# Optimization experiments

Hardware: AMD Instinct MI355X
Metric: run time of the kernel (lower is better)

The kernel has to match this reference:

```python
import jax, jax.numpy as jnp
import numpy as np
import math

B, TSRC, TTGT, DM, DI, H = 2, 2048, 2048, 1024, 1024, 16
DH = DI // H
LN_EPS = 1e-5


def setup_inputs() -> dict:
    key = jax.random.key(0)
    ks = iter(jax.random.split(key, 40))
    def p(*shape):
        return jax.random.normal(next(ks), shape, jnp.float32) * 0.02
    inp = {
        "enc_out_vecs": jax.random.normal(next(ks), (B, TSRC, DM), jnp.float32),
        "output_vecs": jax.random.normal(next(ks), (B, TTGT, DM), jnp.float32),
    }
    for tag in ("dd", "ed"):
        inp["Wq_" + tag] = p(DM, DI); inp["bq_" + tag] = jnp.zeros((DI,), jnp.float32)
        inp["Wk_" + tag] = p(DM, DI); inp["bk_" + tag] = jnp.zeros((DI,), jnp.float32)
        inp["Wv_" + tag] = p(DM, DI); inp["bv_" + tag] = jnp.zeros((DI,), jnp.float32)
        inp["Wo_" + tag] = p(DI, DM); inp["bo_" + tag] = jnp.zeros((DM,), jnp.float32)
        inp["W1_" + tag] = p(DM, 2 * DM); inp["b1_" + tag] = jnp.zeros((2 * DM,), jnp.float32)
        inp["W2_" + tag] = p(2 * DM, DM); inp["b2_" + tag] = jnp.zeros((DM,), jnp.float32)
        inp["g1_" + tag] = jnp.ones((DM,), jnp.float32); inp["be1_" + tag] = jnp.zeros((DM,), jnp.float32)
        inp["g2_" + tag] = jnp.ones((DM,), jnp.float32); inp["be2_" + tag] = jnp.zeros((DM,), jnp.float32)
    return inp


def _ln(x, g, b):
    m = jnp.mean(x, axis=-1, keepdims=True)
    v = jnp.var(x, axis=-1, keepdims=True)
    return (x - m) * jax.lax.rsqrt(v + LN_EPS) * g + b


def _mha(xq, xkv, Wq, bq, Wk, bk, Wv, bv, causal):
    Bb, Tq, _ = xq.shape
    Tk = xkv.shape[1]
    q = (xq @ Wq + bq).reshape(Bb, Tq, H, DH)
    k = (xkv @ Wk + bk).reshape(Bb, Tk, H, DH)
    v = (xkv @ Wv + bv).reshape(Bb, Tk, H, DH)
    s = jnp.einsum("bqhd,bkhd->bhqk", q, k) / math.sqrt(DH)
    if causal:
        mask = jnp.where(jnp.arange(Tk)[None, :] > jnp.arange(Tq)[:, None], -jnp.inf, 0.0)
        s = s + mask
    w = jax.nn.softmax(s, axis=-1)
    return jnp.einsum("bhqk,bkhd->bqhd", w, v).reshape(Bb, Tq, H * DH)


def reference(enc_out_vecs, output_vecs,
              Wq_dd, bq_dd, Wk_dd, bk_dd, Wv_dd, bv_dd, Wo_dd, bo_dd,
              W1_dd, b1_dd, W2_dd, b2_dd, g1_dd, be1_dd, g2_dd, be2_dd,
              Wq_ed, bq_ed, Wk_ed, bk_ed, Wv_ed, bv_ed, Wo_ed, bo_ed,
              W1_ed, b1_ed, W2_ed, b2_ed, g1_ed, be1_ed, g2_ed, be2_ed):
    # masked self-attention over decoder inputs
    x = output_vecs
    a = _mha(x, x, Wq_dd, bq_dd, Wk_dd, bk_dd, Wv_dd, bv_dd, causal=True)
    x = _ln(a @ Wo_dd + bo_dd + x, g1_dd, be1_dd)
    x = _ln(x + jax.nn.relu(x @ W1_dd + b1_dd) @ W2_dd + b2_dd, g2_dd, be2_dd)
    # cross attention against encoder outputs
    a = _mha(x, enc_out_vecs, Wq_ed, bq_ed, Wk_ed, bk_ed, Wv_ed, bv_ed, causal=False)
    x = _ln(a @ Wo_ed + bo_ed + x, g1_ed, be1_ed)
    x = _ln(jax.nn.relu(x @ W1_ed + b1_ed) @ W2_ed + b2_ed + x, g2_ed, be2_ed)
    return x
```

## Files before the change

### kernel.cpp

```cpp
#include <hip/hip_runtime.h>
#include <stdint.h>

#define DEV __device__ __forceinline__
typedef unsigned short u16;
typedef __attribute__((ext_vector_type(8))) short bf16x8;
typedef __attribute__((ext_vector_type(4))) float f32x4;

#define AS1 __attribute__((address_space(1)))
#define AS3 __attribute__((address_space(3)))
#define WAITVM0 asm volatile("s_waitcnt vmcnt(0)" ::: "memory")
#define QSCALE 0.18033688011112042f

DEV u16 f2bf(float f) {
  union { float f; uint32_t u; } x; x.f = f;
  uint32_t r = x.u + 0x7fffu + ((x.u >> 16) & 1u);
  return (u16)(r >> 16);
}

DEV uint32_t cvt_pk_bf16(float a, float b) {
  uint32_t r;
  asm("v_cvt_pk_bf16_f32 %0, %1, %2" : "=v"(r) : "v"(a), "v"(b));
  return r;
}

__global__ __launch_bounds__(256) void k_cvt2(const float* __restrict__ a, const float* __restrict__ bsrc,
                                              u16* __restrict__ oa, u16* __restrict__ ob, int n4) {
  int i = blockIdx.x * blockDim.x + threadIdx.x;
  const float* s;
  u16* o;
  int k;
  if (i < n4) { s = a; o = oa; k = i; }
  else        { s = bsrc; o = ob; k = i - n4; }
  float4 v = reinterpret_cast<const float4*>(s)[k];
  reinterpret_cast<ushort4*>(o)[k] = make_ushort4(f2bf(v.x), f2bf(v.y), f2bf(v.z), f2bf(v.w));
}

struct WTJob { const float* W; u16* WT; int K, M, msh, start; };
struct WTJobs { WTJob j[12]; };

__global__ void k_wT_all(WTJobs jobs) {
  __shared__ float tile[32][33];
  int b = blockIdx.x;
  int i = 0;
#pragma unroll
  for (int t = 1; t < 12; ++t)
    if (b >= jobs.j[t].start) i = t;
  const WTJob J = jobs.j[i];
  int rel = b - J.start;
  int m0 = (rel & ((1 << J.msh) - 1)) << 5;
  int k0 = (rel >> J.msh) << 5;
  int tx = threadIdx.x, ty = threadIdx.y;
#pragma unroll
  for (int q = 0; q < 4; ++q)
    tile[ty + q * 8][tx] = J.W[(size_t)(k0 + ty + q * 8) * J.M + m0 + tx];
  __syncthreads();
#pragma unroll
  for (int q = 0; q < 4; ++q)
    J.WT[(size_t)(m0 + ty + q * 8) * J.K + k0 + tx] = f2bf(tile[tx][ty + q * 8]);
}

template<int R>
DEV void stage_tile(const u16* __restrict__ g, int strideElems, u16* lds, int tid, int wv) {
#pragma unroll
  for (int t = 0; t < R / 32; ++t) {
    int idx = t * 256 + tid;
    int row = idx >> 3;
    int b = (idx & 7) << 4;
    int sb = b ^ ((row & 7) << 4);
    const char* src = (const char*)g + (size_t)row * strideElems * 2 + sb;
    char* dst = (char*)lds + (size_t)(t * 256 + wv * 64) * 16;
    __builtin_amdgcn_global_load_lds((const AS1 void*)src, (AS3 void*)dst, 16, 0, 0);
  }
}

DEV bf16x8 lds_frag(const u16* lds, int row, int kel) {
  int off = row * 128 + ((kel * 2) ^ ((row & 7) << 4));
  return *(const bf16x8*)((const char*)lds + off);
}

template<int JT, int MODE>
__global__ __launch_bounds__(256) void k_gemm(const u16* __restrict__ A, int lda,
                                              const u16* __restrict__ BT,
                                              const float* __restrict__ bias,
                                              void* __restrict__ C, int ldc, int K) {
  constexpr int BN = JT * 32;
  __shared__ __align__(16) u16 A_lds[2][128 * 64];
  __shared__ __align__(16) u16 B_lds[2][BN * 64];
  const int tid = threadIdx.x, lane = tid & 63, wv = tid >> 6;
  const int wm = wv >> 1, wn = wv & 1;
  const int nwg = gridDim.x * gridDim.y;
  const int flat = blockIdx.y * gridDim.x + blockIdx.x;
  const int sw = (flat & 7) * (nwg >> 3) + (flat >> 3);
  const int bx = sw % gridDim.x, by = sw / gridDim.x;
  const int bm0 = by * 128, bn0 = bx * BN;
  const int lr = lane & 15, lk = (lane >> 4) * 8, r0 = (lane >> 4) * 4;

  f32x4 acc[4][JT];
#pragma unroll
  for (int i = 0; i < 4; ++i)
#pragma unroll
    for (int j = 0; j < JT; ++j) acc[i][j] = f32x4{0.f, 0.f, 0.f, 0.f};

  stage_tile<128>(A + (size_t)bm0 * lda, lda, A_lds[0], tid, wv);
  stage_tile<BN>(BT + (size_t)bn0 * K, K, B_lds[0], tid, wv);
  WAITVM0;
  __builtin_amdgcn_s_barrier();

  int cur = 0;
  for (int k0 = 0; k0 < K; k0 += 64) {
    if (k0 + 64 < K) {
      stage_tile<128>(A + (size_t)bm0 * lda + k0 + 64, lda, A_lds[cur ^ 1], tid, wv);
      stage_tile<BN>(BT + (size_t)bn0 * K + k0 + 64, K, B_lds[cur ^ 1], tid, wv);
    }
#pragma unroll
    for (int kk = 0; kk < 2; ++kk) {
      bf16x8 af[4], bfr[JT];
#pragma unroll
      for (int i = 0; i < 4; ++i) af[i] = lds_frag(A_lds[cur], wm * 64 + i * 16 + lr, kk * 32 + lk);
#pragma unroll
      for (int j = 0; j < JT; ++j) bfr[j] = lds_frag(B_lds[cur], wn * (JT * 16) + j * 16 + lr, kk * 32 + lk);
#pragma unroll
      for (int i = 0; i < 4; ++i)
#pragma unroll
        for (int j = 0; j < JT; ++j)
          acc[i][j] = __builtin_amdgcn_mfma_f32_16x16x32_bf16(af[i], bfr[j], acc[i][j], 0, 0, 0);
    }
    WAITVM0;
    __builtin_amdgcn_s_barrier();
    cur ^= 1;
  }

#pragma unroll
  for (int j = 0; j < JT; ++j) {
    int col = bn0 + wn * (JT * 16) + j * 16 + lr;
    float bv = bias[col];
#pragma unroll
    for (int i = 0; i < 4; ++i) {
      int rowb = bm0 + wm * 64 + i * 16 + r0;
      if constexpr (MODE == 0) {
#pragma unroll
        for (int r = 0; r < 4; ++r)
          ((float*)C)[(size_t)(rowb + r) * ldc + col] = acc[i][j][r] + bv;
      } else {
#pragma unroll
        for (int r = 0; r < 4; ++r) {
          float v = fmaxf(acc[i][j][r] + bv, 0.f);
          ((u16*)C)[(size_t)(rowb + r) * ldc + col] = f2bf(v);
        }
      }
    }
  }
}

__global__ __launch_bounds__(256) void k_qkv(const u16* __restrict__ Aq, const u16* __restrict__ Akv,
                                             const u16* __restrict__ BT,
                                             const float* __restrict__ bq, const float* __restrict__ bk,
                                             const float* __restrict__ bv,
                                             u16* __restrict__ Qb, u16* __restrict__ Kb,
                                             u16* __restrict__ Vt, int K) {
  __shared__ __align__(16) u16 A_lds[2][128 * 64];
  __shared__ __align__(16) u16 B_lds[2][64 * 64];
  const int tid = threadIdx.x, lane = tid & 63, wv = tid >> 6;
  const int wm = wv >> 1, wn = wv & 1;
  const int nwg = gridDim.x * gridDim.y;
  const int flat = blockIdx.y * gridDim.x + blockIdx.x;
  const int sw = (flat & 7) * (nwg >> 3) + (flat >> 3);
  const int bx = sw % gridDim.x, by = sw / gridDim.x;
  const int bm0 = by * 128, bn0 = bx * 64;
  const int seg = bn0 >> 10;
  const u16* A = (seg == 0) ? Aq : Akv;
  const int lr = lane & 15, lk = (lane >> 4) * 8, r0 = (lane >> 4) * 4;

  f32x4 acc[4][2];
#pragma unroll
  for (int i = 0; i < 4; ++i)
#pragma unroll
    for (int j = 0; j < 2; ++j) acc[i][j] = f32x4{0.f, 0.f, 0.f, 0.f};

  stage_tile<128>(A + (size_t)bm0 * K, K, A_lds[0], tid, wv);
  stage_tile<64>(BT + (size_t)bn0 * K, K, B_lds[0], tid, wv);
  WAITVM0;
  __builtin_amdgcn_s_barrier();

  int cur = 0;
  for (int k0 = 0; k0 < K; k0 += 64) {
    if (k0 + 64 < K) {
      stage_tile<128>(A + (size_t)bm0 * K + k0 + 64, K, A_lds[cur ^ 1], tid, wv);
      stage_tile<64>(BT + (size_t)bn0 * K + k0 + 64, K, B_lds[cur ^ 1], tid, wv);
    }
#pragma unroll
    for (int kk = 0; kk < 2; ++kk) {
      bf16x8 af[4], bfr[2];
#pragma unroll
      for (int i = 0; i < 4; ++i) af[i] = lds_frag(A_lds[cur], wm * 64 + i * 16 + lr, kk * 32 + lk);
#pragma unroll
      for (int j = 0; j < 2; ++j) bfr[j] = lds_frag(B_lds[cur], wn * 32 + j * 16 + lr, kk * 32 + lk);
#pragma unroll
      for (int i = 0; i < 4; ++i)
#pragma unroll
        for (int j = 0; j < 2; ++j)
          acc[i][j] = __builtin_amdgcn_mfma_f32_16x16x32_bf16(af[i], bfr[j], acc[i][j], 0, 0, 0);
    }
    WAITVM0;
    __builtin_amdgcn_s_barrier();
    cur ^= 1;
  }

#pragma unroll
  for (int j = 0; j < 2; ++j) {
    int col = bn0 + wn * 32 + j * 16 + lr;
    int cl = col & 1023;
#pragma unroll
    for (int i = 0; i < 4; ++i) {
      int rowb = bm0 + wm * 64 + i * 16 + r0;
      if (seg == 0) {
        float bb = bq[cl];
#pragma unroll
        for (int r = 0; r < 4; ++r)
          Qb[(size_t)(rowb + r) * 1024 + cl] = f2bf((acc[i][j][r] + bb) * QSCALE);
      } else if (seg == 1) {
        float bb = bk[cl];
#pragma unroll
        for (int r = 0; r < 4; ++r)
          Kb[(size_t)(rowb + r) * 1024 + cl] = f2bf(acc[i][j][r] + bb);
      } else {
        float bb = bv[cl];
        int bidx = rowb >> 11, t = rowb & 2047;
        ushort4 o = make_ushort4(f2bf(acc[i][j][0] + bb), f2bf(acc[i][j][1] + bb),
                                 f2bf(acc[i][j][2] + bb), f2bf(acc[i][j][3] + bb));
        *reinterpret_cast<ushort4*>(&Vt[((size_t)bidx * 1024 + cl) * 2048 + t]) = o;
      }
    }
  }
}

__global__ __launch_bounds__(256) void k_ln(const float* __restrict__ Rm, const float* __restrict__ X,
                                            const float* __restrict__ g, const float* __restrict__ be,
                                            float* __restrict__ Y, u16* __restrict__ Yb) {
  int row = blockIdx.x;
  size_t base4 = (size_t)row * 256;
  int t = threadIdx.x;
  float4 a = reinterpret_cast<const float4*>(Rm)[base4 + t];
  float4 x = reinterpret_cast<const float4*>(X)[base4 + t];
  float v0 = a.x + x.x, v1 = a.y + x.y, v2 = a.z + x.z, v3 = a.w + x.w;
  float s = v0 + v1 + v2 + v3;
  float ss = v0 * v0 + v1 * v1 + v2 * v2 + v3 * v3;
#pragma unroll
  for (int m = 1; m < 64; m <<= 1) { s += __shfl_xor(s, m); ss += __shfl_xor(ss, m); }
  __shared__ float red[8];
  int wv = t >> 6;
  if ((t & 63) == 0) { red[wv] = s; red[4 + wv] = ss; }
  __syncthreads();
  s = red[0] + red[1] + red[2] + red[3];
  ss = red[4] + red[5] + red[6] + red[7];
  float mean = s * (1.f / 1024.f);
  float var = ss * (1.f / 1024.f) - mean * mean;
  float rstd = rsqrtf(var + 1e-5f);
  float4 gv = reinterpret_cast<const float4*>(g)[t];
  float4 bv = reinterpret_cast<const float4*>(be)[t];
  float o0 = (v0 - mean) * rstd * gv.x + bv.x;
  float o1 = (v1 - mean) * rstd * gv.y + bv.y;
  float o2 = (v2 - mean) * rstd * gv.z + bv.z;
  float o3 = (v3 - mean) * rstd * gv.w + bv.w;
  reinterpret_cast<float4*>(Y)[base4 + t] = make_float4(o0, o1, o2, o3);
  if (Yb) {
    ushort4 ob = make_ushort4(f2bf(o0), f2bf(o1), f2bf(o2), f2bf(o3));
    reinterpret_cast<ushort4*>(Yb)[base4 + t] = ob;
  }
}

template<bool CAUSAL>
__global__ __launch_bounds__(256) void k_attn(const u16* __restrict__ Q, const u16* __restrict__ Kg,
                                              const u16* __restrict__ Vt, u16* __restrict__ O,
                                              float* __restrict__ OP0, float* __restrict__ OP1,
                                              float* __restrict__ L0, float* __restrict__ L1, int T) {
  __shared__ __align__(16) u16 K_lds[2][64 * 64];
  __shared__ __align__(16) u16 V_lds[2][64 * 64];
  __shared__ __align__(16) u16 p_lds[4][16 * 64];
  const int tid = threadIdx.x, lane = tid & 63, wv = tid >> 6;
  const int h = blockIdx.y, b = blockIdx.z;
  const int lq = lane & 15, g = lane >> 4;
  const int swz = (lq & 7) << 4;
  const int fb0 = lq * 128 + ((g * 16) ^ swz);
  const int fb1 = lq * 128 + ((g * 16 + 64) ^ swz);
  const size_t qkbase = ((size_t)b * T) * 1024 + h * 64;
  const size_t vbase = ((size_t)b * 1024 + h * 64) * T;

  int qx, st, en;
  if constexpr (CAUSAL) {
    qx = 31 - (blockIdx.x >> 1);
    const int s = blockIdx.x & 1;
    const int ntf = qx + 1, half = (ntf + 1) >> 1;
    st = s ? half : 0;
    en = s ? ntf : half;
  } else {
    qx = blockIdx.x;
    st = 0;
    en = T >> 6;
  }
  const int nt = en - st;
  const int qw = qx * 64 + wv * 16;

  bf16x8 aq0, aq1;
  {
    const u16* qp_ = Q + qkbase + (size_t)(qw + lq) * 1024 + g * 8;
    aq0 = *reinterpret_cast<const bf16x8*>(qp_);
    aq1 = *reinterpret_cast<const bf16x8*>(qp_ + 32);
  }

  const int srow = tid >> 3;
  const int ssb = ((tid & 7) << 4) ^ ((srow & 7) << 4);
  const char* ksrc = (const char*)(Kg + qkbase) + (size_t)srow * 2048 + ssb + (size_t)st * 131072;
  const char* vsrc = (const char*)(Vt + vbase) + (size_t)srow * ((size_t)T * 2) + ssb + (size_t)st * 128;
  const int vstep2 = T * 64;
  const uint32_t doff = (uint32_t)((tid & 192) << 4);

  auto stage = [&](const char* kp, const char* vp, int buf) {
    char* kd = (char*)K_lds[buf] + doff;
    char* vd = (char*)V_lds[buf] + doff;
    __builtin_amdgcn_global_load_lds((const AS1 void*)kp, (AS3 void*)kd, 16, 0, 0);
    __builtin_amdgcn_global_load_lds((const AS1 void*)(kp + 65536), (AS3 void*)(kd + 4096), 16, 0, 0);
    __builtin_amdgcn_global_load_lds((const AS1 void*)vp, (AS3 void*)vd, 16, 0, 0);
    __builtin_amdgcn_global_load_lds((const AS1 void*)(vp + vstep2), (AS3 void*)(vd + 4096), 16, 0, 0);
  };

  f32x4 acc[4];
  float lsum = 0.f;
#pragma unroll
  for (int j = 0; j < 4; ++j) acc[j] = f32x4{0.f, 0.f, 0.f, 0.f};

  char* pw = (char*)p_lds[wv];

  if (nt > 0) {
    stage(ksrc, vsrc, 0);
    WAITVM0;
    __builtin_amdgcn_s_barrier();
    ksrc += 131072;
    vsrc += 128;

    int cur = 0;
    for (int it = st; it < en; ++it) {
      if (it + 1 < en) {
        stage(ksrc, vsrc, cur ^ 1);
        ksrc += 131072;
        vsrc += 128;
      }
      const char* kb = (const char*)K_lds[cur];
      const char* vb = (const char*)V_lds[cur];
      f32x4 st_[4];
      __builtin_amdgcn_s_setprio(1);
#pragma unroll
      for (int j = 0; j < 4; ++j) {
        bf16x8 bk0 = *reinterpret_cast<const bf16x8*>(kb + fb0 + j * 2048);
        bf16x8 bk1 = *reinterpret_cast<const bf16x8*>(kb + fb1 + j * 2048);
        f32x4 t0 = f32x4{0.f, 0.f, 0.f, 0.f};
        t0 = __builtin_amdgcn_mfma_f32_16x16x32_bf16(bk0, aq0, t0, 0, 0, 0);
        t0 = __builtin_amdgcn_mfma_f32_16x16x32_bf16(bk1, aq1, t0, 0, 0, 0);
        st_[j] = t0;
      }
      __builtin_amdgcn_s_setprio(0);
      uint32_t pk[8];
      if (CAUSAL && it == qx) {
        const int qrow = qw + lq, kv0 = it << 6;
#pragma unroll
        for (int j = 0; j < 4; ++j) {
          float p0 = __builtin_exp2f(st_[j][0]);
          float p1 = __builtin_exp2f(st_[j][1]);
          float p2 = __builtin_exp2f(st_[j][2]);
          float p3 = __builtin_exp2f(st_[j][3]);
          int kvb = kv0 + j * 16 + g * 4;
          p0 = (kvb > qrow) ? 0.f : p0;
          p1 = (kvb + 1 > qrow) ? 0.f : p1;
          p2 = (kvb + 2 > qrow) ? 0.f : p2;
          p3 = (kvb + 3 > qrow) ? 0.f : p3;
          lsum += (p0 + p1) + (p2 + p3);
          pk[2 * j] = cvt_pk_bf16(p0, p1);
          pk[2 * j + 1] = cvt_pk_bf16(p2, p3);
        }
      } else {
#pragma unroll
        for (int j = 0; j < 4; ++j) {
          float p0 = __builtin_exp2f(st_[j][0]);
          float p1 = __builtin_exp2f(st_[j][1]);
          float p2 = __builtin_exp2f(st_[j][2]);
          float p3 = __builtin_exp2f(st_[j][3]);
          lsum += (p0 + p1) + (p2 + p3);
          pk[2 * j] = cvt_pk_bf16(p0, p1);
          pk[2 * j + 1] = cvt_pk_bf16(p2, p3);
        }
      }
#pragma unroll
      for (int j = 0; j < 4; ++j)
        *reinterpret_cast<uint2*>(pw + lq * 128 + ((j * 32 + g * 8) ^ swz)) =
            make_uint2(pk[2 * j], pk[2 * j + 1]);
      bf16x8 pf0 = *reinterpret_cast<const bf16x8*>(pw + fb0);
      bf16x8 pf1 = *reinterpret_cast<const bf16x8*>(pw + fb1);
      __builtin_amdgcn_s_setprio(1);
#pragma unroll
      for (int j2 = 0; j2 < 4; ++j2) {
        bf16x8 v0 = *reinterpret_cast<const bf16x8*>(vb + fb0 + j2 * 2048);
        bf16x8 v1 = *reinterpret_cast<const bf16x8*>(vb + fb1 + j2 * 2048);
        acc[j2] = __builtin_amdgcn_mfma_f32_16x16x32_bf16(v0, pf0, acc[j2], 0, 0, 0);
        acc[j2] = __builtin_amdgcn_mfma_f32_16x16x32_bf16(v1, pf1, acc[j2], 0, 0, 0);
      }
      __builtin_amdgcn_s_setprio(0);
      WAITVM0;
      __builtin_amdgcn_s_barrier();
      cur ^= 1;
    }
  }

  lsum += __shfl_xor(lsum, 16);
  lsum += __shfl_xor(lsum, 32);
  if constexpr (CAUSAL) {
    float* OP = (blockIdx.x & 1) ? OP1 : OP0;
    float* Lp = (blockIdx.x & 1) ? L1 : L0;
    const int row = (b * 16 + h) * 2048 + qw + lq;
    float* pr = OP + (size_t)row * 64;
#pragma unroll
    for (int j2 = 0; j2 < 4; ++j2)
      *reinterpret_cast<f32x4*>(pr + j2 * 16 + g * 4) = acc[j2];
    if (g == 0) Lp[row] = lsum;
  } else {
    float inv = 1.f / lsum;
    size_t rb = qkbase + (size_t)(qw + lq) * 1024;
#pragma unroll
    for (int j2 = 0; j2 < 4; ++j2) {
      ushort4 o = make_ushort4(f2bf(acc[j2][0] * inv), f2bf(acc[j2][1] * inv),
                               f2bf(acc[j2][2] * inv), f2bf(acc[j2][3] * inv));
      *reinterpret_cast<ushort4*>(&O[rb + j2 * 16 + g * 4]) = o;
    }
  }
}

__global__ __launch_bounds__(256) void k_amrg(const float* __restrict__ P0, const float* __restrict__ P1,
                                              const float* __restrict__ L0, const float* __restrict__ L1,
                                              u16* __restrict__ Ab) {
  int i = blockIdx.x * 256 + threadIdx.x;
  int row = i >> 4, d4 = (i & 15) << 2;
  f32x4 a = *reinterpret_cast<const f32x4*>(&P0[(size_t)row * 64 + d4]);
  f32x4 c = *reinterpret_cast<const f32x4*>(&P1[(size_t)row * 64 + d4]);
  float inv = 1.f / (L0[row] + L1[row]);
  int bh = row >> 11, q = row & 2047, bb = bh >> 4, hh = bh & 15;
  size_t dst = ((size_t)(bb * 2048 + q)) * 1024 + hh * 64 + d4;
  ushort4 o = make_ushort4(f2bf((a[0] + c[0]) * inv), f2bf((a[1] + c[1]) * inv),
                           f2bf((a[2] + c[2]) * inv), f2bf((a[3] + c[3]) * inv));
  *reinterpret_cast<ushort4*>(&Ab[dst]) = o;
}

extern "C" void kernel_launch(void* const* d_in, const int* in_sizes, int n_in,
                              void* d_out, int out_size, void* d_ws, size_t ws_size,
                              hipStream_t stream) {
  const int T = 2048;
  const float* enc = (const float*)d_in[0];
  const float* outv = (const float*)d_in[1];
  auto F = [&](int i) { return (const float*)d_in[i]; };

  size_t off = 0;
  auto alloc = [&](size_t bytes) {
    void* p = (char*)d_ws + off;
    off += (bytes + 255) & ~(size_t)255;
    return p;
  };

  const int tdK[12] = {1024, 1024, 1024, 1024, 1024, 2048, 1024, 1024, 1024, 1024, 1024, 2048};
  const int tdM[12] = {1024, 1024, 1024, 1024, 2048, 1024, 1024, 1024, 1024, 1024, 2048, 1024};
  const int tdIdx[12] = {2, 4, 6, 8, 10, 12, 18, 20, 22, 24, 26, 28};
  u16* WT_[12];
  for (int i = 0; i < 12; ++i) WT_[i] = (u16*)alloc((size_t)tdK[i] * tdM[i] * 2);

  u16* Xb0 = (u16*)alloc(4096ull * 1024 * 2);
  u16* Eb = (u16*)alloc(4096ull * 1024 * 2);
  u16* Qb = (u16*)alloc(4096ull * 1024 * 2);
  u16* Kb = (u16*)alloc(4096ull * 1024 * 2);
  u16* Vt = (u16*)alloc(4096ull * 1024 * 2);
  u16* Ab = (u16*)alloc(4096ull * 1024 * 2);
  u16* Hb = (u16*)alloc(4096ull * 2048 * 2);
  u16* Xbc = (u16*)alloc(4096ull * 1024 * 2);
  float* Rf = (float*)alloc(4096ull * 1024 * 4);
  float* Xfa = (float*)alloc(4096ull * 1024 * 4);
  float* Xfb = (float*)alloc(4096ull * 1024 * 4);
  float* Lsum = (float*)alloc(2ull * 65536 * 4);

  k_cvt2<<<8192, 256, 0, stream>>>(outv, enc, Xb0, Eb, 4096 * 1024 / 4);

  WTJobs jobs;
  int start = 0;
  for (int i = 0; i < 12; ++i) {
    int msh = (tdM[i] == 2048) ? 6 : 5;
    jobs.j[i] = {F(tdIdx[i]), WT_[i], tdK[i], tdM[i], msh, start};
    start += (tdM[i] >> 5) * (tdK[i] >> 5);
  }
  k_wT_all<<<start, dim3(32, 8), 0, stream>>>(jobs);

  float* OP0 = Rf;
  float* OP1 = (float*)Hb;
  float* L0 = Lsum;
  float* L1 = Lsum + 65536;

  dim3 gq(48, 32);
  dim3 g1k(16, 32);
  dim3 g2k(16, 32);
  dim3 gac(64, 16, 2);
  dim3 gan(32, 16, 2);

  k_qkv<<<gq, 256, 0, stream>>>(Xb0, Xb0, WT_[0], F(3), F(5), F(7), Qb, Kb, Vt, 1024);
  k_attn<true><<<gac, 256, 0, stream>>>(Qb, Kb, Vt, Ab, OP0, OP1, L0, L1, T);
  k_amrg<<<4096, 256, 0, stream>>>(OP0, OP1, L0, L1, Ab);
  k_gemm<2, 0><<<g1k, 256, 0, stream>>>(Ab, 1024, WT_[3], F(9), Rf, 1024, 1024);
  k_ln<<<4096, 256, 0, stream>>>(Rf, outv, F(14), F(15), Xfa, Xbc);
  k_gemm<4, 2><<<g2k, 256, 0, stream>>>(Xbc, 1024, WT_[4], F(11), Hb, 2048, 1024);
  k_gemm<2, 0><<<g1k, 256, 0, stream>>>(Hb, 2048, WT_[5], F(13), Rf, 1024, 2048);
  k_ln<<<4096, 256, 0, stream>>>(Rf, Xfa, F(16), F(17), Xfb, Xbc);

  k_qkv<<<gq, 256, 0, stream>>>(Xbc, Eb, WT_[6], F(19), F(21), F(23), Qb, Kb, Vt, 1024);
  k_attn<false><<<gan, 256, 0, stream>>>(Qb, Kb, Vt, Ab, OP0, OP1, L0, L1, T);
  k_gemm<2, 0><<<g1k, 256, 0, stream>>>(Ab, 1024, WT_[9], F(25), Rf, 1024, 1024);
  k_ln<<<4096, 256, 0, stream>>>(Rf, Xfb, F(30), F(31), Xfa, Xbc);
  k_gemm<4, 2><<<g2k, 256, 0, stream>>>(Xbc, 1024, WT_[10], F(27), Hb, 2048, 1024);
  k_gemm<2, 0><<<g1k, 256, 0, stream>>>(Hb, 2048, WT_[11], F(29), Rf, 1024, 2048);
  k_ln<<<4096, 256, 0, stream>>>(Rf, Xfa, F(32), F(33), (float*)d_out, (u16*)nullptr);
}
```

Baseline: 452.1 us.

## Use 128-row query tiles with 8 waves and triple-buffered K/V in attention

Each attention block now covers 128 query rows using 512 threads (8 waves), so every K/V tile staged in shared memory serves twice as many query rows. The grid is halved to match. The K/V staging goes from double to triple buffering, with a partial vmcnt wait so loads run two tiles ahead. In the causal kernel, waves whose rows lie entirely before a tile skip it, and the split point and diagonal tile are recomputed per wave. The costs are more shared memory per block, fewer blocks, and load imbalance between the waves of a block near the diagonal.

```diff
diff --git a/kernel.cpp b/kernel.cpp
--- a/kernel.cpp
+++ b/kernel.cpp
@@ -270,13 +270,13 @@
 }
 
 template<bool CAUSAL>
-__global__ __launch_bounds__(256) void k_attn(const u16* __restrict__ Q, const u16* __restrict__ Kg,
+__global__ __launch_bounds__(512) void k_attn(const u16* __restrict__ Q, const u16* __restrict__ Kg,
                                               const u16* __restrict__ Vt, u16* __restrict__ O,
                                               float* __restrict__ OP0, float* __restrict__ OP1,
                                               float* __restrict__ L0, float* __restrict__ L1, int T) {
-  __shared__ __align__(16) u16 K_lds[2][64 * 64];
-  __shared__ __align__(16) u16 V_lds[2][64 * 64];
-  __shared__ __align__(16) u16 p_lds[4][16 * 64];
+  __shared__ __align__(16) u16 K_lds[3][64 * 64];
+  __shared__ __align__(16) u16 V_lds[3][64 * 64];
+  __shared__ __align__(16) u16 p_lds[8][16 * 64];
   const int tid = threadIdx.x, lane = tid & 63, wv = tid >> 6;
   const int h = blockIdx.y, b = blockIdx.z;
   const int lq = lane & 15, g = lane >> 4;
@@ -288,9 +288,9 @@
 
   int qx, st, en;
   if constexpr (CAUSAL) {
-    qx = 31 - (blockIdx.x >> 1);
+    qx = 15 - (blockIdx.x >> 1);
     const int s = blockIdx.x & 1;
-    const int ntf = qx + 1, half = (ntf + 1) >> 1;
+    const int ntf = 2 * qx + 2, half = qx + 1;
     st = s ? half : 0;
     en = s ? ntf : half;
   } else {
@@ -298,8 +298,8 @@
     st = 0;
     en = T >> 6;
   }
-  const int nt = en - st;
-  const int qw = qx * 64 + wv * 16;
+  const int qw = qx * 128 + wv * 16;
+  const int dtile = qw >> 6;
 
   bf16x8 aq0, aq1;
   {
@@ -312,16 +312,13 @@
   const int ssb = ((tid & 7) << 4) ^ ((srow & 7) << 4);
   const char* ksrc = (const char*)(Kg + qkbase) + (size_t)srow * 2048 + ssb + (size_t)st * 131072;
   const char* vsrc = (const char*)(Vt + vbase) + (size_t)srow * ((size_t)T * 2) + ssb + (size_t)st * 128;
-  const int vstep2 = T * 64;
-  const uint32_t doff = (uint32_t)((tid & 192) << 4);
-
-  auto stage = [&](const char* kp, const char* vp, int buf) {
-    char* kd = (char*)K_lds[buf] + doff;
-    char* vd = (char*)V_lds[buf] + doff;
-    __builtin_amdgcn_global_load_lds((const AS1 void*)kp, (AS3 void*)kd, 16, 0, 0);
-    __builtin_amdgcn_global_load_lds((const AS1 void*)(kp + 65536), (AS3 void*)(kd + 4096), 16, 0, 0);
-    __builtin_amdgcn_global_load_lds((const AS1 void*)vp, (AS3 void*)vd, 16, 0, 0);
-    __builtin_amdgcn_global_load_lds((const AS1 void*)(vp + vstep2), (AS3 void*)(vd + 4096), 16, 0, 0);
+  const uint32_t doff = (uint32_t)(wv << 10);
+
+  auto stage = [&](int buf) {
+    __builtin_amdgcn_global_load_lds((const AS1 void*)ksrc, (AS3 void*)((char*)K_lds[buf] + doff), 16, 0, 0);
+    __builtin_amdgcn_global_load_lds((const AS1 void*)vsrc, (AS3 void*)((char*)V_lds[buf] + doff), 16, 0, 0);
+    ksrc += 131072;
+    vsrc += 128;
   };
 
   f32x4 acc[4];
@@ -331,83 +328,88 @@
 
   char* pw = (char*)p_lds[wv];
 
-  if (nt > 0) {
-    stage(ksrc, vsrc, 0);
+  auto qstep = [&](bool domask, int kv0, const char* kb, const char* vb) {
+    f32x4 st_[4];
+    __builtin_amdgcn_s_setprio(1);
+#pragma unroll
+    for (int j = 0; j < 4; ++j) {
+      bf16x8 bk0 = *reinterpret_cast<const bf16x8*>(kb + fb0 + j * 2048);
+      bf16x8 bk1 = *reinterpret_cast<const bf16x8*>(kb + fb1 + j * 2048);
+      f32x4 t0 = f32x4{0.f, 0.f, 0.f, 0.f};
+      t0 = __builtin_amdgcn_mfma_f32_16x16x32_bf16(bk0, aq0, t0, 0, 0, 0);
+      t0 = __builtin_amdgcn_mfma_f32_16x16x32_bf16(bk1, aq1, t0, 0, 0, 0);
+      st_[j] = t0;
+    }
+    __builtin_amdgcn_s_setprio(0);
+    uint32_t pk[8];
+    if (domask) {
+      const int qrow = qw + lq;
+#pragma unroll
+      for (int j = 0; j < 4; ++j) {
+        float p0 = __builtin_exp2f(st_[j][0]);
+        float p1 = __builtin_exp2f(st_[j][1]);
+        float p2 = __builtin_exp2f(st_[j][2]);
+        float p3 = __builtin_exp2f(st_[j][3]);
+        int kvb = kv0 + j * 16 + g * 4;
+        p0 = (kvb > qrow) ? 0.f : p0;
+        p1 = (kvb + 1 > qrow) ? 0.f : p1;
+        p2 = (kvb + 2 > qrow) ? 0.f : p2;
+        p3 = (kvb + 3 > qrow) ? 0.f : p3;
+        lsum += (p0 + p1) + (p2 + p3);
+        pk[2 * j] = cvt_pk_bf16(p0, p1);
+        pk[2 * j + 1] = cvt_pk_bf16(p2, p3);
+      }
+    } else {
+#pragma unroll
+      for (int j = 0; j < 4; ++j) {
+        float p0 = __builtin_exp2f(st_[j][0]);
+        float p1 = __builtin_exp2f(st_[j][1]);
+        float p2 = __builtin_exp2f(st_[j][2]);
+        float p3 = __builtin_exp2f(st_[j][3]);
+        lsum += (p0 + p1) + (p2 + p3);
+        pk[2 * j] = cvt_pk_bf16(p0, p1);
+        pk[2 * j + 1] = cvt_pk_bf16(p2, p3);
+      }
+    }
+#pragma unroll
+    for (int j = 0; j < 4; ++j)
+      *reinterpret_cast<uint2*>(pw + lq * 128 + ((j * 32 + g * 8) ^ swz)) =
+          make_uint2(pk[2 * j], pk[2 * j + 1]);
+    bf16x8 pf0 = *reinterpret_cast<const bf16x8*>(pw + fb0);
+    bf16x8 pf1 = *reinterpret_cast<const bf16x8*>(pw + fb1);
+    __builtin_amdgcn_s_setprio(1);
+#pragma unroll
+    for (int j2 = 0; j2 < 4; ++j2) {
+      bf16x8 v0 = *reinterpret_cast<const bf16x8*>(vb + fb0 + j2 * 2048);
+      bf16x8 v1 = *reinterpret_cast<const bf16x8*>(vb + fb1 + j2 * 2048);
+      acc[j2] = __builtin_amdgcn_mfma_f32_16x16x32_bf16(v0, pf0, acc[j2], 0, 0, 0);
+      acc[j2] = __builtin_amdgcn_mfma_f32_16x16x32_bf16(v1, pf1, acc[j2], 0, 0, 0);
+    }
+    __builtin_amdgcn_s_setprio(0);
+  };
+
+  stage(0);
+  if (st + 1 < en) {
+    stage(1);
+    asm volatile("s_waitcnt vmcnt(2)" ::: "memory");
+  } else {
     WAITVM0;
+  }
+  __builtin_amdgcn_s_barrier();
+
+  for (int it = st; it < en; ++it) {
+    const int idx = it - st;
+    if (it + 2 < en) stage((idx + 2) % 3);
+    const char* kb = (const char*)K_lds[idx % 3];
+    const char* vb = (const char*)V_lds[idx % 3];
+    if (!CAUSAL || it <= dtile)
+      qstep(CAUSAL && it == dtile, it << 6, kb, vb);
+    if (it + 2 < en) {
+      asm volatile("s_waitcnt vmcnt(2)" ::: "memory");
+    } else {
+      WAITVM0;
+    }
     __builtin_amdgcn_s_barrier();
-    ksrc += 131072;
-    vsrc += 128;
-
-    int cur = 0;
-    for (int it = st; it < en; ++it) {
-      if (it + 1 < en) {
-        stage(ksrc, vsrc, cur ^ 1);
-        ksrc += 131072;
-        vsrc += 128;
-      }
-      const char* kb = (const char*)K_lds[cur];
-      const char* vb = (const char*)V_lds[cur];
-      f32x4 st_[4];
-      __builtin_amdgcn_s_setprio(1);
-#pragma unroll
-      for (int j = 0; j < 4; ++j) {
-        bf16x8 bk0 = *reinterpret_cast<const bf16x8*>(kb + fb0 + j * 2048);
-        bf16x8 bk1 = *reinterpret_cast<const bf16x8*>(kb + fb1 + j * 2048);
-        f32x4 t0 = f32x4{0.f, 0.f, 0.f, 0.f};
-        t0 = __builtin_amdgcn_mfma_f32_16x16x32_bf16(bk0, aq0, t0, 0, 0, 0);
-        t0 = __builtin_amdgcn_mfma_f32_16x16x32_bf16(bk1, aq1, t0, 0, 0, 0);
-        st_[j] = t0;
-      }
-      __builtin_amdgcn_s_setprio(0);
-      uint32_t pk[8];
-      if (CAUSAL && it == qx) {
-        const int qrow = qw + lq, kv0 = it << 6;
-#pragma unroll
-        for (int j = 0; j < 4; ++j) {
-          float p0 = __builtin_exp2f(st_[j][0]);
-          float p1 = __builtin_exp2f(st_[j][1]);
-          float p2 = __builtin_exp2f(st_[j][2]);
-          float p3 = __builtin_exp2f(st_[j][3]);
-          int kvb = kv0 + j * 16 + g * 4;
-          p0 = (kvb > qrow) ? 0.f : p0;
-          p1 = (kvb + 1 > qrow) ? 0.f : p1;
-          p2 = (kvb + 2 > qrow) ? 0.f : p2;
-          p3 = (kvb + 3 > qrow) ? 0.f : p3;
-          lsum += (p0 + p1) + (p2 + p3);
-          pk[2 * j] = cvt_pk_bf16(p0, p1);
-          pk[2 * j + 1] = cvt_pk_bf16(p2, p3);
-        }
-      } else {
-#pragma unroll
-        for (int j = 0; j < 4; ++j) {
-          float p0 = __builtin_exp2f(st_[j][0]);
-          float p1 = __builtin_exp2f(st_[j][1]);
-          float p2 = __builtin_exp2f(st_[j][2]);
-          float p3 = __builtin_exp2f(st_[j][3]);
-          lsum += (p0 + p1) + (p2 + p3);
-          pk[2 * j] = cvt_pk_bf16(p0, p1);
-          pk[2 * j + 1] = cvt_pk_bf16(p2, p3);
-        }
-      }
-#pragma unroll
-      for (int j = 0; j < 4; ++j)
-        *reinterpret_cast<uint2*>(pw + lq * 128 + ((j * 32 + g * 8) ^ swz)) =
-            make_uint2(pk[2 * j], pk[2 * j + 1]);
-      bf16x8 pf0 = *reinterpret_cast<const bf16x8*>(pw + fb0);
-      bf16x8 pf1 = *reinterpret_cast<const bf16x8*>(pw + fb1);
-      __builtin_amdgcn_s_setprio(1);
-#pragma unroll
-      for (int j2 = 0; j2 < 4; ++j2) {
-        bf16x8 v0 = *reinterpret_cast<const bf16x8*>(vb + fb0 + j2 * 2048);
-        bf16x8 v1 = *reinterpret_cast<const bf16x8*>(vb + fb1 + j2 * 2048);
-        acc[j2] = __builtin_amdgcn_mfma_f32_16x16x32_bf16(v0, pf0, acc[j2], 0, 0, 0);
-        acc[j2] = __builtin_amdgcn_mfma_f32_16x16x32_bf16(v1, pf1, acc[j2], 0, 0, 0);
-      }
-      __builtin_amdgcn_s_setprio(0);
-      WAITVM0;
-      __builtin_amdgcn_s_barrier();
-      cur ^= 1;
-    }
   }
 
   lsum += __shfl_xor(lsum, 16);
@@ -501,11 +503,11 @@
   dim3 gq(48, 32);
   dim3 g1k(16, 32);
   dim3 g2k(16, 32);
-  dim3 gac(64, 16, 2);
-  dim3 gan(32, 16, 2);
+  dim3 gac(32, 16, 2);
+  dim3 gan(16, 16, 2);
 
   k_qkv<<<gq, 256, 0, stream>>>(Xb0, Xb0, WT_[0], F(3), F(5), F(7), Qb, Kb, Vt, 1024);
-  k_attn<true><<<gac, 256, 0, stream>>>(Qb, Kb, Vt, Ab, OP0, OP1, L0, L1, T);
+  k_attn<true><<<gac, 512, 0, stream>>>(Qb, Kb, Vt, Ab, OP0, OP1, L0, L1, T);
   k_amrg<<<4096, 256, 0, stream>>>(OP0, OP1, L0, L1, Ab);
   k_gemm<2, 0><<<g1k, 256, 0, stream>>>(Ab, 1024, WT_[3], F(9), Rf, 1024, 1024);
   k_ln<<<4096, 256, 0, stream>>>(Rf, outv, F(14), F(15), Xfa, Xbc);
@@ -514,7 +516,7 @@
   k_ln<<<4096, 256, 0, stream>>>(Rf, Xfa, F(16), F(17), Xfb, Xbc);
 
   k_qkv<<<gq, 256, 0, stream>>>(Xbc, Eb, WT_[6], F(19), F(21), F(23), Qb, Kb, Vt, 1024);
-  k_attn<false><<<gan, 256, 0, stream>>>(Qb, Kb, Vt, Ab, OP0, OP1, L0, L1, T);
+  k_attn<false><<<gan, 512, 0, stream>>>(Qb, Kb, Vt, Ab, OP0, OP1, L0, L1, T);
   k_gemm<2, 0><<<g1k, 256, 0, stream>>>(Ab, 1024, WT_[9], F(25), Rf, 1024, 1024);
   k_ln<<<4096, 256, 0, stream>>>(Rf, Xfb, F(30), F(31), Xfa, Xbc);
   k_gemm<4, 2><<<g2k, 256, 0, stream>>>(Xbc, 1024, WT_[10], F(27), Hb, 2048, 1024);
```

Result: no change. 444.5 us (-1.7%).
